# Performance work log

Measured on AMD Instinct MI355X. Metric: run time of the kernel, lower is better.

## Reference

```python
import jax, jax.numpy as jnp
import numpy as np

EMBED_DIM = 512
NUM_HEADS = 8
HEAD_DIM = EMBED_DIM // NUM_HEADS
SCALE = HEAD_DIM ** -0.5
TEMP = 1.0


def setup_inputs() -> dict:
    key = jax.random.key(0)
    ks = jax.random.split(key, 12)
    B, N, Nk, C = 4, 2048, 2048, EMBED_DIM
    s = C ** -0.5
    return {
        "x": jax.random.normal(ks[0], (B, N, C), jnp.float32),
        "y": jax.random.normal(ks[1], (B, Nk, C), jnp.float32),
        "z": jax.random.normal(ks[2], (B, Nk, C), jnp.float32),
        "Wq": jax.random.normal(ks[3], (C, C), jnp.float32) * s,
        "bq": jnp.zeros((C,), jnp.float32),
        "Wk": jax.random.normal(ks[4], (C, C), jnp.float32) * s,
        "bk": jnp.zeros((C,), jnp.float32),
        "Wv": jax.random.normal(ks[5], (C, C), jnp.float32) * s,
        "bv": jnp.zeros((C,), jnp.float32),
        "Wo": jax.random.normal(ks[6], (C, C), jnp.float32) * s,
        "bo": jnp.zeros((C,), jnp.float32),
    }


def reference(x, y, z, Wq, bq, Wk, bk, Wv, bv, Wo, bo):
    B, N, C = x.shape
    Nk = y.shape[1]
    H, D = NUM_HEADS, HEAD_DIM

    def split_heads(t, L):
        return t.reshape(B, L, H, D).transpose(0, 2, 1, 3)  # [B,H,L,D]

    q = split_heads(x @ Wq.T + bq, N)
    k = split_heads(y @ Wk.T + bk, Nk)
    v = split_heads(z @ Wv.T + bv, Nk)

    # [B,H,N,Nk] logits, scaled
    logits = jnp.einsum("bhnd,bhkd->bhnk", q, k) * SCALE

    # Gumbel-softmax (soft, tau=TEMP) with a fixed noise key
    gkey = jax.random.key(42)
    gumbels = jax.random.gumbel(gkey, logits.shape, logits.dtype)
    attn = jax.nn.softmax((logits + gumbels) / TEMP, axis=-1)

    out = jnp.einsum("bhnk,bhkd->bhnd", attn, v)
    out = out.transpose(0, 2, 1, 3).reshape(B, N, C)
    return out @ Wo.T + bo
```

## Files before the change

kernel.cpp:

```cpp
#include <hip/hip_runtime.h>
#include <hip/hip_bf16.h>
#include <stdint.h>

#define Bdim 4
#define Hdim 8
#define Ndim 2048
#define Cdim 512
#define Ddim 64
#define SCALE_F 0.125f
#define KSPLIT 4
#define LOG2E 1.44269504f
#define QSCALE_F (SCALE_F * LOG2E)

typedef __bf16 bf16_t;
typedef __bf16 bf16x8 __attribute__((ext_vector_type(8)));
typedef float f32x4 __attribute__((ext_vector_type(4)));

__device__ __forceinline__ float gumbel_pfac(uint32_t flat) {
  const uint32_t k0 = 0u, k1 = 42u, k2 = 0x1BD11BDAu ^ 0u ^ 42u;
  uint32_t x0 = 0u;
  uint32_t x1 = flat;
  x0 += k0; x1 += k1;
#define TF_R(r) { x0 += x1; x1 = __builtin_rotateleft32(x1, r); x1 ^= x0; }
#define TF_R4A TF_R(13) TF_R(15) TF_R(26) TF_R(6)
#define TF_R4B TF_R(17) TF_R(29) TF_R(16) TF_R(24)
  TF_R4A  x0 += k1; x1 += k2 + 1u;
  TF_R4B  x0 += k2; x1 += k0 + 2u;
  TF_R4A  x0 += k0; x1 += k1 + 3u;
  TF_R4B  x0 += k1; x1 += k2 + 4u;
  TF_R4A  x0 += k2; x1 += k0 + 5u;
#undef TF_R4B
#undef TF_R4A
#undef TF_R
  uint32_t bits = x0 ^ x1;
  uint32_t mant;
  asm("v_alignbit_b32 %0, %1, %2, 9" : "=v"(mant) : "s"(127u), "v"(bits));
  float u = __uint_as_float(mant) - 1.0f;
  return -__builtin_amdgcn_rcpf(__builtin_amdgcn_logf(u));
}

__global__ void cvt_f32_bf16(const float* __restrict__ in,
                             bf16_t* __restrict__ out, int n8) {
  int i = blockIdx.x * blockDim.x + threadIdx.x;
  if (i < n8) {
    const float4* p = (const float4*)in + (size_t)i * 2;
    float4 a = p[0], b = p[1];
    union { bf16_t h[8]; uint4 u; } pk;
    pk.h[0] = (bf16_t)a.x; pk.h[1] = (bf16_t)a.y;
    pk.h[2] = (bf16_t)a.z; pk.h[3] = (bf16_t)a.w;
    pk.h[4] = (bf16_t)b.x; pk.h[5] = (bf16_t)b.y;
    pk.h[6] = (bf16_t)b.z; pk.h[7] = (bf16_t)b.w;
    *((uint4*)out + i) = pk.u;
  }
}

__device__ __forceinline__ void gemm_core(const bf16_t* __restrict__ A,
                                          const bf16_t* __restrict__ W,
                                          int m0, int n0,
                                          bf16_t* As, bf16_t* Ws,
                                          f32x4 (&acc)[4][4]) {
  const int t = threadIdx.x;
  const int wave = t >> 6, lane = t & 63;
  const int ln = lane & 15, qd = lane >> 4;
  const int wm = wave >> 1, wn = wave & 1;

#pragma unroll
  for (int i = 0; i < 4; i++)
#pragma unroll
    for (int j = 0; j < 4; j++) acc[i][j] = (f32x4){0.f, 0.f, 0.f, 0.f};

  for (int kt = 0; kt < Cdim / 64; ++kt) {
#pragma unroll
    for (int it = 0; it < 4; ++it) {
      int vec = it * 256 + t;
      int row = vec >> 3, c8 = (vec & 7) * 8;
      *(bf16x8*)&As[row * 72 + c8] =
          *(const bf16x8*)&A[(size_t)(m0 + row) * Cdim + kt * 64 + c8];
      *(bf16x8*)&Ws[row * 72 + c8] =
          *(const bf16x8*)&W[(size_t)(n0 + row) * Cdim + kt * 64 + c8];
    }
    __syncthreads();
#pragma unroll
    for (int ks = 0; ks < 2; ++ks) {
      bf16x8 af[4], bfr[4];
#pragma unroll
      for (int i = 0; i < 4; i++)
        af[i] = *(const bf16x8*)&As[(wm * 64 + i * 16 + ln) * 72 + ks * 32 + qd * 8];
#pragma unroll
      for (int j = 0; j < 4; j++)
        bfr[j] = *(const bf16x8*)&Ws[(wn * 64 + j * 16 + ln) * 72 + ks * 32 + qd * 8];
#pragma unroll
      for (int i = 0; i < 4; i++)
#pragma unroll
        for (int j = 0; j < 4; j++)
          acc[i][j] = __builtin_amdgcn_mfma_f32_16x16x32_bf16(af[i], bfr[j],
                                                              acc[i][j], 0, 0, 0);
    }
    __syncthreads();
  }
}

__global__ __launch_bounds__(256, 2)
void qkv_gemm_kernel(const bf16_t* __restrict__ xb, const bf16_t* __restrict__ yb,
                     const bf16_t* __restrict__ zb, const bf16_t* __restrict__ wqb,
                     const bf16_t* __restrict__ wkb, const bf16_t* __restrict__ wvb,
                     const float* __restrict__ bq, const float* __restrict__ bk,
                     const float* __restrict__ bv, bf16_t* __restrict__ qo,
                     bf16_t* __restrict__ ko, bf16_t* __restrict__ vo) {
  __shared__ bf16_t As[128 * 72];
  __shared__ bf16_t Ws[128 * 72];
  const int sel = blockIdx.z;
  const bf16_t* A = sel == 0 ? xb : (sel == 1 ? yb : zb);
  const bf16_t* W = sel == 0 ? wqb : (sel == 1 ? wkb : wvb);
  const float* bias = sel == 0 ? bq : (sel == 1 ? bk : bv);
  bf16_t* O = sel == 0 ? qo : (sel == 1 ? ko : vo);
  const float mul = sel == 0 ? QSCALE_F : 1.0f;
  const int m0 = blockIdx.y * 128, n0 = blockIdx.x * 128;

  f32x4 acc[4][4];
  gemm_core(A, W, m0, n0, As, Ws, acc);

  const int t = threadIdx.x;
  const int wave = t >> 6, lane = t & 63;
  const int ln = lane & 15, qd = lane >> 4;
  const int wm = wave >> 1, wn = wave & 1;
#pragma unroll
  for (int i = 0; i < 4; i++)
#pragma unroll
    for (int j = 0; j < 4; j++)
#pragma unroll
      for (int r = 0; r < 4; r++) {
        int grow = m0 + wm * 64 + i * 16 + qd * 4 + r;
        int gcol = n0 + wn * 64 + j * 16 + ln;
        float val = (acc[i][j][r] + bias[gcol]) * mul;
        int b = grow >> 11, n = grow & 2047;
        int h = gcol >> 6, d = gcol & 63;
        O[(((size_t)b * Hdim + h) * Ndim + n) * Ddim + d] = (bf16_t)val;
      }
}

__global__ __launch_bounds__(256, 2)
void out_gemm_kernel(const bf16_t* __restrict__ ab, const bf16_t* __restrict__ wob,
                     const float* __restrict__ bo, float* __restrict__ out) {
  __shared__ bf16_t As[128 * 72];
  __shared__ bf16_t Ws[128 * 72];
  const int m0 = blockIdx.y * 128, n0 = blockIdx.x * 128;
  f32x4 acc[4][4];
  gemm_core(ab, wob, m0, n0, As, Ws, acc);

  const int t = threadIdx.x;
  const int wave = t >> 6, lane = t & 63;
  const int ln = lane & 15, qd = lane >> 4;
  const int wm = wave >> 1, wn = wave & 1;
#pragma unroll
  for (int i = 0; i < 4; i++)
#pragma unroll
    for (int j = 0; j < 4; j++)
#pragma unroll
      for (int r = 0; r < 4; r++) {
        int grow = m0 + wm * 64 + i * 16 + qd * 4 + r;
        int gcol = n0 + wn * 64 + j * 16 + ln;
        out[(size_t)grow * Cdim + gcol] = acc[i][j][r] + bo[gcol];
      }
}

__global__ __launch_bounds__(256, 4)
void attn_kernel(const bf16_t* __restrict__ qb, const bf16_t* __restrict__ kb,
                 const bf16_t* __restrict__ vb, bf16_t* __restrict__ part_o,
                 float* __restrict__ part_l) {
  __shared__ bf16_t KPs[64 * 72];
  __shared__ bf16_t Vt[64 * 72];

  const int t = threadIdx.x;
  const int wave = t >> 6, lane = t & 63;
  const int ln = lane & 15, qd = lane >> 4;
  const int qtile = blockIdx.x;
  const int bh = blockIdx.y;
  const int z = blockIdx.z;
  const int qbase = qtile * 64;
  const int kt_lo = z * (Ndim / 64 / KSPLIT);
  const int kt_hi = kt_lo + (Ndim / 64 / KSPLIT);

  const bf16_t* Qg = qb + (size_t)bh * Ndim * Ddim;
  const bf16_t* Kg = kb + (size_t)bh * Ndim * Ddim;
  const bf16_t* Vg = vb + (size_t)bh * Ndim * Ddim;

  const bf16_t* Qrow = Qg + (size_t)(qbase + wave * 16 + ln) * Ddim;
  bf16x8 qf0 = *(const bf16x8*)&Qrow[qd * 8];
  bf16x8 qf1 = *(const bf16x8*)&Qrow[32 + qd * 8];

  const bf16_t one_h = (bf16_t)1.0f;
  bf16x8 ones;
#pragma unroll
  for (int i = 0; i < 8; i++) ones[i] = one_h;

  const int row0 = t >> 3,        c80 = (t & 7) * 8;
  const int row1 = (256 + t) >> 3, c81 = ((256 + t) & 7) * 8;
  const int swz0 = ((row0 >> 3) ^ (c80 >> 3)) * 8 + (row0 & 7);
  const int swz1 = ((row1 >> 3) ^ (c81 >> 3)) * 8 + (row1 & 7);

  bf16x8 kr0 = *(const bf16x8*)&Kg[(size_t)(kt_lo * 64 + row0) * Ddim + c80];
  bf16x8 kr1 = *(const bf16x8*)&Kg[(size_t)(kt_lo * 64 + row1) * Ddim + c81];
  bf16x8 vr0 = *(const bf16x8*)&Vg[(size_t)(kt_lo * 64 + row0) * Ddim + c80];
  bf16x8 vr1 = *(const bf16x8*)&Vg[(size_t)(kt_lo * 64 + row1) * Ddim + c81];

  f32x4 l_acc = (f32x4){0.f, 0.f, 0.f, 0.f};
  f32x4 o_acc[4];
#pragma unroll
  for (int j = 0; j < 4; j++) o_acc[j] = (f32x4){0.f, 0.f, 0.f, 0.f};

  const uint32_t flat_bh = (uint32_t)bh << 22;

  for (int kt = kt_lo; kt < kt_hi; ++kt) {
    *(bf16x8*)&KPs[row0 * 72 + c80] = kr0;
    *(bf16x8*)&KPs[row1 * 72 + c81] = kr1;
#pragma unroll
    for (int jj = 0; jj < 8; jj++) Vt[(c80 + jj) * 72 + swz0] = vr0[jj];
#pragma unroll
    for (int jj = 0; jj < 8; jj++) Vt[(c81 + jj) * 72 + swz1] = vr1[jj];
    __syncthreads();

    if (kt + 1 < kt_hi) {
      kr0 = *(const bf16x8*)&Kg[(size_t)((kt + 1) * 64 + row0) * Ddim + c80];
      kr1 = *(const bf16x8*)&Kg[(size_t)((kt + 1) * 64 + row1) * Ddim + c81];
      vr0 = *(const bf16x8*)&Vg[(size_t)((kt + 1) * 64 + row0) * Ddim + c80];
      vr1 = *(const bf16x8*)&Vg[(size_t)((kt + 1) * 64 + row1) * Ddim + c81];
    }

    f32x4 s[4];
#pragma unroll
    for (int j = 0; j < 4; j++) s[j] = (f32x4){0.f, 0.f, 0.f, 0.f};
#pragma unroll
    for (int j = 0; j < 4; j++) {
      bf16x8 bk0 = *(const bf16x8*)&KPs[(j * 16 + ln) * 72 + qd * 8];
      bf16x8 bk1 = *(const bf16x8*)&KPs[(j * 16 + ln) * 72 + 32 + qd * 8];
      s[j] = __builtin_amdgcn_mfma_f32_16x16x32_bf16(qf0, bk0, s[j], 0, 0, 0);
      s[j] = __builtin_amdgcn_mfma_f32_16x16x32_bf16(qf1, bk1, s[j], 0, 0, 0);
    }
    __syncthreads();

#pragma unroll
    for (int r = 0; r < 4; r++) {
      int qrow = qbase + wave * 16 + qd * 4 + r;
      uint32_t fbase = flat_bh + ((uint32_t)qrow << 11) + (uint32_t)(kt * 64 + ln);
#pragma unroll
      for (int j = 0; j < 4; j++) {
        float pf = gumbel_pfac(fbase + j * 16);
        float pv = __builtin_amdgcn_exp2f(s[j][r]) * pf;
        KPs[(wave * 16 + qd * 4 + r) * 72 + j * 16 + ln] = (bf16_t)pv;
      }
    }

#pragma unroll
    for (int ks = 0; ks < 2; ++ks) {
      bf16x8 af = *(const bf16x8*)&KPs[(wave * 16 + ln) * 72 + ks * 32 + qd * 8];
      l_acc = __builtin_amdgcn_mfma_f32_16x16x32_bf16(af, ones, l_acc, 0, 0, 0);
#pragma unroll
      for (int j = 0; j < 4; j++) {
        int d = j * 16 + ln;
        bf16x8 bv8 = *(const bf16x8*)&Vt[d * 72 + (((ks * 4 + qd) ^ (d >> 3)) << 3)];
        o_acc[j] = __builtin_amdgcn_mfma_f32_16x16x32_bf16(af, bv8, o_acc[j], 0, 0, 0);
      }
    }
    __syncthreads();
  }

  const int pidx = ((bh << 5) | qtile) * KSPLIT + z;
  bf16_t* po = part_o + (size_t)pidx * 64 * 64;
  float* pl = part_l + (size_t)pidx * 64;

  if (ln == 0) {
#pragma unroll
    for (int r = 0; r < 4; r++) pl[wave * 16 + qd * 4 + r] = l_acc[r];
  }
#pragma unroll
  for (int j = 0; j < 4; j++)
#pragma unroll
    for (int r = 0; r < 4; r++) {
      int row = wave * 16 + qd * 4 + r;
      int col = j * 16 + ln;
      po[row * 64 + col] = (bf16_t)o_acc[j][r];
    }
}

__global__ __launch_bounds__(256, 8)
void attn_combine(const bf16_t* __restrict__ part_o,
                  const float* __restrict__ part_l, bf16_t* __restrict__ ab) {
  const int blk = blockIdx.x;
  const int bh = blk >> 5, qtile = blk & 31;
  const int t = threadIdx.x;
  const int row = t >> 2, c0 = (t & 3) * 16;

  float l = 0.f;
#pragma unroll
  for (int zz = 0; zz < KSPLIT; zz++)
    l += part_l[(size_t)(blk * KSPLIT + zz) * 64 + row];
  const float linv = 1.0f / l;

  float acc[16];
#pragma unroll
  for (int i = 0; i < 16; i++) acc[i] = 0.f;
#pragma unroll
  for (int zz = 0; zz < KSPLIT; zz++) {
    const bf16_t* po =
        part_o + (size_t)(blk * KSPLIT + zz) * 64 * 64 + row * 64 + c0;
    bf16x8 a0 = *(const bf16x8*)&po[0];
    bf16x8 a1 = *(const bf16x8*)&po[8];
#pragma unroll
    for (int i = 0; i < 8; i++) { acc[i] += (float)a0[i]; acc[8 + i] += (float)a1[i]; }
  }

  const int b = bh >> 3, h = bh & 7;
  bf16_t* dst = ab + ((size_t)b * Ndim + qtile * 64 + row) * Cdim + h * 64 + c0;
  union { bf16_t h8[8]; uint4 u; } pk0, pk1;
#pragma unroll
  for (int i = 0; i < 8; i++) {
    pk0.h8[i] = (bf16_t)(acc[i] * linv);
    pk1.h8[i] = (bf16_t)(acc[8 + i] * linv);
  }
  *(uint4*)&dst[0] = pk0.u;
  *(uint4*)&dst[8] = pk1.u;
}

extern "C" void kernel_launch(void* const* d_in, const int* in_sizes, int n_in,
                              void* d_out, int out_size, void* d_ws, size_t ws_size,
                              hipStream_t stream) {
  const float* x  = (const float*)d_in[0];
  const float* y  = (const float*)d_in[1];
  const float* z  = (const float*)d_in[2];
  const float* Wq = (const float*)d_in[3];
  const float* bq = (const float*)d_in[4];
  const float* Wk = (const float*)d_in[5];
  const float* bk = (const float*)d_in[6];
  const float* Wv = (const float*)d_in[7];
  const float* bv = (const float*)d_in[8];
  const float* Wo = (const float*)d_in[9];
  const float* bo = (const float*)d_in[10];
  float* out = (float*)d_out;

  bf16_t* base = (bf16_t*)d_ws;
  const size_t NBIG = (size_t)Bdim * Ndim * Cdim;
  const size_t NW   = (size_t)Cdim * Cdim;
  bf16_t* xb  = base;
  bf16_t* yb  = xb + NBIG;
  bf16_t* zb  = yb + NBIG;
  bf16_t* wqb = zb + NBIG;
  bf16_t* wkb = wqb + NW;
  bf16_t* wvb = wkb + NW;
  bf16_t* wob = wvb + NW;
  bf16_t* qb  = wob + NW;
  bf16_t* kb  = qb + NBIG;
  bf16_t* vb  = kb + NBIG;
  bf16_t* ab  = vb + NBIG;
  bf16_t* part_o = ab + NBIG;
  float* part_l = (float*)(part_o + (size_t)1024 * KSPLIT * 64 * 64);

  int n8b = (int)(NBIG / 8), n8w = (int)(NW / 8);
  cvt_f32_bf16<<<n8b / 256, 256, 0, stream>>>(x, xb, n8b);
  cvt_f32_bf16<<<n8b / 256, 256, 0, stream>>>(y, yb, n8b);
  cvt_f32_bf16<<<n8b / 256, 256, 0, stream>>>(z, zb, n8b);
  cvt_f32_bf16<<<n8w / 256, 256, 0, stream>>>(Wq, wqb, n8w);
  cvt_f32_bf16<<<n8w / 256, 256, 0, stream>>>(Wk, wkb, n8w);
  cvt_f32_bf16<<<n8w / 256, 256, 0, stream>>>(Wv, wvb, n8w);
  cvt_f32_bf16<<<n8w / 256, 256, 0, stream>>>(Wo, wob, n8w);

  qkv_gemm_kernel<<<dim3(Cdim / 128, (Bdim * Ndim) / 128, 3), 256, 0, stream>>>(
      xb, yb, zb, wqb, wkb, wvb, bq, bk, bv, qb, kb, vb);

  attn_kernel<<<dim3(Ndim / 64, Bdim * Hdim, KSPLIT), 256, 0, stream>>>(
      qb, kb, vb, part_o, part_l);

  attn_combine<<<dim3(1024), 256, 0, stream>>>(part_o, part_l, ab);

  out_gemm_kernel<<<dim3(Cdim / 128, (Bdim * Ndim) / 128), 256, 0, stream>>>(
      ab, wob, bo, out);
}
```

Measured before the change: 432.8 us.

## Split P into its own LDS buffer and precompute next tile's Gumbel noise

Gives the probability tile its own shared-memory buffer instead of reusing the K buffer, which removes one block barrier per iteration. The Gumbel noise for the next key tile is now computed at the end of the current iteration, before the closing barrier, so the ALU-heavy Threefry hashing can overlap with MFMA work in flight. The hash's initial key add is folded into a precomputed base. The cost is extra LDS per block (a third 64x72 bf16 buffer) and 16 extra live float registers, which may reduce occupancy.

```diff
diff --git a/kernel.cpp b/kernel.cpp
--- a/kernel.cpp
+++ b/kernel.cpp
@@ -16,11 +16,10 @@
 typedef __bf16 bf16x8 __attribute__((ext_vector_type(8)));
 typedef float f32x4 __attribute__((ext_vector_type(4)));
 
-__device__ __forceinline__ float gumbel_pfac(uint32_t flat) {
+__device__ __forceinline__ float gumbel_pfac(uint32_t x1init) {
   const uint32_t k0 = 0u, k1 = 42u, k2 = 0x1BD11BDAu ^ 0u ^ 42u;
   uint32_t x0 = 0u;
-  uint32_t x1 = flat;
-  x0 += k0; x1 += k1;
+  uint32_t x1 = x1init;
 #define TF_R(r) { x0 += x1; x1 = __builtin_rotateleft32(x1, r); x1 ^= x0; }
 #define TF_R4A TF_R(13) TF_R(15) TF_R(26) TF_R(6)
 #define TF_R4B TF_R(17) TF_R(29) TF_R(16) TF_R(24)
@@ -39,6 +38,14 @@
   return -__builtin_amdgcn_rcpf(__builtin_amdgcn_logf(u));
 }
 
+__device__ __forceinline__ void gumbel_tile(uint32_t base, float (&pf)[4][4]) {
+#pragma unroll
+  for (int r = 0; r < 4; r++)
+#pragma unroll
+    for (int j = 0; j < 4; j++)
+      pf[r][j] = gumbel_pfac(base + ((uint32_t)r << 11) + (uint32_t)(j * 16));
+}
+
 __global__ void cvt_f32_bf16(const float* __restrict__ in,
                              bf16_t* __restrict__ out, int n8) {
   int i = blockIdx.x * blockDim.x + threadIdx.x;
@@ -168,8 +175,9 @@
 void attn_kernel(const bf16_t* __restrict__ qb, const bf16_t* __restrict__ kb,
                  const bf16_t* __restrict__ vb, bf16_t* __restrict__ part_o,
                  float* __restrict__ part_l) {
-  __shared__ bf16_t KPs[64 * 72];
+  __shared__ bf16_t Ks[64 * 72];
   __shared__ bf16_t Vt[64 * 72];
+  __shared__ bf16_t Ps[64 * 72];
 
   const int t = threadIdx.x;
   const int wave = t >> 6, lane = t & 63;
@@ -209,11 +217,16 @@
 #pragma unroll
   for (int j = 0; j < 4; j++) o_acc[j] = (f32x4){0.f, 0.f, 0.f, 0.f};
 
-  const uint32_t flat_bh = (uint32_t)bh << 22;
+  const uint32_t base_rc = ((uint32_t)bh << 22) +
+                           ((uint32_t)(qbase + wave * 16 + qd * 4) << 11) +
+                           (uint32_t)ln + 42u;
+
+  float pf[4][4];
+  gumbel_tile(base_rc + (uint32_t)(kt_lo * 64), pf);
 
   for (int kt = kt_lo; kt < kt_hi; ++kt) {
-    *(bf16x8*)&KPs[row0 * 72 + c80] = kr0;
-    *(bf16x8*)&KPs[row1 * 72 + c81] = kr1;
+    *(bf16x8*)&Ks[row0 * 72 + c80] = kr0;
+    *(bf16x8*)&Ks[row1 * 72 + c81] = kr1;
 #pragma unroll
     for (int jj = 0; jj < 8; jj++) Vt[(c80 + jj) * 72 + swz0] = vr0[jj];
 #pragma unroll
@@ -232,28 +245,23 @@
     for (int j = 0; j < 4; j++) s[j] = (f32x4){0.f, 0.f, 0.f, 0.f};
 #pragma unroll
     for (int j = 0; j < 4; j++) {
-      bf16x8 bk0 = *(const bf16x8*)&KPs[(j * 16 + ln) * 72 + qd * 8];
-      bf16x8 bk1 = *(const bf16x8*)&KPs[(j * 16 + ln) * 72 + 32 + qd * 8];
+      bf16x8 bk0 = *(const bf16x8*)&Ks[(j * 16 + ln) * 72 + qd * 8];
+      bf16x8 bk1 = *(const bf16x8*)&Ks[(j * 16 + ln) * 72 + 32 + qd * 8];
       s[j] = __builtin_amdgcn_mfma_f32_16x16x32_bf16(qf0, bk0, s[j], 0, 0, 0);
       s[j] = __builtin_amdgcn_mfma_f32_16x16x32_bf16(qf1, bk1, s[j], 0, 0, 0);
     }
-    __syncthreads();
-
-#pragma unroll
-    for (int r = 0; r < 4; r++) {
-      int qrow = qbase + wave * 16 + qd * 4 + r;
-      uint32_t fbase = flat_bh + ((uint32_t)qrow << 11) + (uint32_t)(kt * 64 + ln);
+
+#pragma unroll
+    for (int r = 0; r < 4; r++)
 #pragma unroll
       for (int j = 0; j < 4; j++) {
-        float pf = gumbel_pfac(fbase + j * 16);
-        float pv = __builtin_amdgcn_exp2f(s[j][r]) * pf;
-        KPs[(wave * 16 + qd * 4 + r) * 72 + j * 16 + ln] = (bf16_t)pv;
+        float pv = __builtin_amdgcn_exp2f(s[j][r]) * pf[r][j];
+        Ps[(wave * 16 + qd * 4 + r) * 72 + j * 16 + ln] = (bf16_t)pv;
       }
-    }
 
 #pragma unroll
     for (int ks = 0; ks < 2; ++ks) {
-      bf16x8 af = *(const bf16x8*)&KPs[(wave * 16 + ln) * 72 + ks * 32 + qd * 8];
+      bf16x8 af = *(const bf16x8*)&Ps[(wave * 16 + ln) * 72 + ks * 32 + qd * 8];
       l_acc = __builtin_amdgcn_mfma_f32_16x16x32_bf16(af, ones, l_acc, 0, 0, 0);
 #pragma unroll
       for (int j = 0; j < 4; j++) {
@@ -262,6 +270,10 @@
         o_acc[j] = __builtin_amdgcn_mfma_f32_16x16x32_bf16(af, bv8, o_acc[j], 0, 0, 0);
       }
     }
+
+    if (kt + 1 < kt_hi)
+      gumbel_tile(base_rc + (uint32_t)((kt + 1) * 64), pf);
+
     __syncthreads();
   }
 
```

Result: no change. 431.4 us (-0.3%).
